# Kernel optimization log

Hardware: AMD Instinct MI355X
Metric: run time of the kernel (lower is better)

The kernel has to match this reference:

```python
import jax, jax.numpy as jnp
import numpy as np
import math

B, SEQ, E, H, NB, NHYP = 4, 1024, 512, 8, 64, 6
V, HID, NC, ENC = 32000, 2048, 6, 6
DH = E // H


def _pos_encoding(n, e, dtype):
    pos = jnp.arange(n, dtype=dtype)[:, None]
    div = jnp.exp(-jnp.arange(0, e, 2, dtype=dtype) * (math.log(10000.0) / e))
    ang = pos * div  # [n, e/2]
    pe = jnp.zeros((n, e), dtype)
    pe = pe.at[:, 0::2].set(jnp.sin(ang))
    pe = pe.at[:, 1::2].set(jnp.cos(ang))
    return pe


def _layer_norm(x, g, b):
    m = x.mean(-1, keepdims=True)
    v = ((x - m) ** 2).mean(-1, keepdims=True)
    return (x - m) / jnp.sqrt(v + 1e-5) * g + b


def _lsh_attention(x, Wq, bq, Wv, bv, hyper):
    b, n, e = x.shape
    q = x @ Wq + bq
    v = x @ Wv + bv
    q4 = q.reshape(b, n, H, DH)  # [b,n,h,d]
    v4 = v.reshape(b, n, H, DH)
    # bucket hashing: append bias 1, project on hyperplanes, binarize, binary-encode
    aug = jnp.concatenate([q4, jnp.ones((b, n, H, 1), q.dtype)], axis=-1)
    proj = jnp.einsum('bnhe,ey->bnhy', aug, hyper)
    bits = (proj >= 0).astype(q.dtype)
    pows = (2 ** jnp.arange(NHYP)).astype(q.dtype)
    buckets = jnp.einsum('bnhy,y->bnh', bits, pows).astype(jnp.int32)
    bh = buckets.transpose(0, 2, 1)  # [b,h,n]
    qh = q4.transpose(0, 2, 1, 3)  # [b,h,n,d]
    vh = v4.transpose(0, 2, 1, 3)
    scores = jnp.einsum('bhnd,bhmd->bhnm', qh, qh) / math.sqrt(e)
    # torch code zeroes q rows at their OWN bucket and sums q_c @ q_c^T over all
    # NB buckets; that equals scores * (NB - 2 + [bucket_i == bucket_j]) exactly.
    same = bh[:, :, :, None] == bh[:, :, None, :]
    count = (NB - 2 + same.astype(jnp.int32)).astype(scores.dtype)
    attn = jax.nn.softmax(scores * count, axis=-1)
    out = jnp.einsum('bhnm,bhmd->bhnd', attn, vh)
    return out.transpose(0, 2, 1, 3).reshape(b, n, e)


def setup_inputs() -> dict:
    key = jax.random.key(0)
    ks = jax.random.split(key, 16)
    s = 0.02
    emb = jax.random.normal(ks[0], (V, E), jnp.float32) * s
    emb = emb.at[V - 1].set(0.0)  # padding_idx row
    return dict(
        inputs=jax.random.randint(ks[1], (B, SEQ), 0, V),
        emb=emb,
        gamma=jnp.ones((E,), jnp.float32),
        beta=jnp.zeros((E,), jnp.float32),
        Wq=jax.random.normal(ks[2], (E, E), jnp.float32) * s,
        bq=jnp.zeros((E,), jnp.float32),
        Wv=jax.random.normal(ks[3], (E, E), jnp.float32) * s,
        bv=jnp.zeros((E,), jnp.float32),
        hyper=jax.random.normal(ks[4], (DH + 1, NHYP), jnp.float32),
        W1=jax.random.normal(ks[5], (E, HID), jnp.float32) * s,
        b1=jnp.zeros((HID,), jnp.float32),
        W2=jax.random.normal(ks[6], (HID, E), jnp.float32) * s,
        b2=jnp.zeros((E,), jnp.float32),
        Wm=jax.random.normal(ks[7], (E * SEQ, NC), jnp.float32) * 0.002,
        bm=jnp.zeros((NC,), jnp.float32),
    )


def reference(inputs, emb, gamma, beta, Wq, bq, Wv, bv, hyper, W1, b1, W2, b2, Wm, bm):
    x = emb[inputs]  # [B, SEQ, E]
    x = x + _pos_encoding(x.shape[1], x.shape[2], x.dtype)
    for _ in range(ENC):  # shared weights across encoders
        a = _lsh_attention(x, Wq, bq, Wv, bv, hyper)
        x = _layer_norm(a, gamma, beta)
        x = jax.nn.relu(x @ W1 + b1) @ W2 + b2 + x
        x = _layer_norm(x, gamma, beta)
    x = x.reshape(x.shape[0], -1)
    return x @ Wm + bm  # [B, NC]
```

## Files before the change

### kernel.cpp

```cpp
#include <hip/hip_runtime.h>
#include <hip/hip_bf16.h>
#include <math.h>

#define B_    4
#define SEQ_  1024
#define E_    512
#define H_    8
#define DH_   64
#define NHYP_ 6
#define HID_  2048
#define NC_   6
#define ENC_  6
#define BH_   (B_*H_)
#define NTOK_ 4096
#define NCAT_ 1088

typedef __attribute__((ext_vector_type(8))) short short8;
typedef __attribute__((ext_vector_type(4))) float f32x4;

static __device__ __forceinline__ float wave_rsum(float v){
#pragma unroll
  for(int o=32;o;o>>=1) v += __shfl_down(v,o,64);
  return v;
}
static __device__ __forceinline__ ushort f2b(float v){
  __hip_bfloat16 h = __float2bfloat16(v);
  return *(ushort*)&h;
}
static __device__ __forceinline__ float b2f(ushort u){
  unsigned int x = ((unsigned int)u) << 16;
  return *(float*)&x;
}
static __device__ __forceinline__ void gload16(const void* g, void* l){
  __builtin_amdgcn_global_load_lds(
      (const __attribute__((address_space(1))) void*)g,
      (__attribute__((address_space(3))) void*)l,
      16, 0, 0);
}

__global__ void embed_pe_kernel(const int* __restrict__ inp, const float* __restrict__ emb,
                                float* __restrict__ x, ushort* __restrict__ xh,
                                unsigned int* __restrict__ MaxN){
  int row = blockIdx.x;
  if(blockIdx.x==0 && threadIdx.x<32) MaxN[threadIdx.x] = 0u;
  int s = row & (SEQ_-1);
  int idx = inp[row];
  const float* er = emb + (size_t)idx*E_;
  float* xr = x + (size_t)row*E_;
  ushort* hr = xh + (size_t)row*E_;
  for(int c=threadIdx.x;c<E_;c+=blockDim.x){
    int i = c>>1;
    float div = expf(-(float)i * 0.0359778920780319646f);
    float ang = (float)s * div;
    float pe = (c&1) ? cosf(ang) : sinf(ang);
    float v = er[c] + pe;
    xr[c] = v;
    hr[c] = f2b(v);
  }
}

__global__ __launch_bounds__(256) void prep_kernel(
    const float* __restrict__ Wq, const float* __restrict__ Wv,
    const float* __restrict__ W1, const float* __restrict__ W2,
    const float* __restrict__ bq, const float* __restrict__ bv,
    const float* __restrict__ hyper,
    ushort* __restrict__ WcatT, ushort* __restrict__ W1T,
    ushort* __restrict__ W2T, float* __restrict__ bcat)
{
  int bid = blockIdx.x;
  if(bid < 2560){
    const float* W; ushort* Wt; int K, N, tile;
    if(bid < 256){       W=Wq; Wt=WcatT;                    K=512;  N=512;  tile=bid; }
    else if(bid < 512){  W=Wv; Wt=WcatT+(size_t)512*512;    K=512;  N=512;  tile=bid-256; }
    else if(bid < 1536){ W=W1; Wt=W1T;                      K=512;  N=2048; tile=bid-512; }
    else {               W=W2; Wt=W2T;                      K=2048; N=512;  tile=bid-1536; }
    int tpr = N >> 5;
    int n0 = (tile % tpr)*32, k0 = (tile / tpr)*32;
    __shared__ float T[32][33];
    int tx = threadIdx.x & 31, ty = threadIdx.x >> 5;
#pragma unroll
    for(int i=0;i<32;i+=8) T[ty+i][tx] = W[(size_t)(k0+ty+i)*N + n0+tx];
    __syncthreads();
#pragma unroll
    for(int i=0;i<32;i+=8)
      Wt[(size_t)(n0+ty+i)*K + k0+tx] = f2b(T[tx][ty+i]);
  } else if(bid < 2688){
    int t = (bid-2560)*256 + threadIdx.x;
    int c = t >> 9, k = t & 511;
    float s = 0.f;
    if(c < 48){
      int h = c/6, y = c%6;
      const float* wr = Wq + (size_t)k*E_ + h*DH_;
      for(int d=0;d<DH_;++d) s += wr[d]*hyper[d*NHYP_+y];
    }
    WcatT[(size_t)(1024+c)*E_ + k] = f2b(s);
  } else {
    int t = (bid-2688)*256 + threadIdx.x;
    if(t >= NCAT_) return;
    float v;
    if(t < 512) v = bq[t];
    else if(t < 1024) v = bv[t-512];
    else if(t < 1072){
      int c = t - 1024, h = c/6, y = c%6;
      float s = hyper[DH_*NHYP_ + y];
      for(int d=0;d<DH_;++d) s += bq[h*DH_+d]*hyper[d*NHYP_+y];
      v = s;
    } else v = 0.f;
    bcat[t] = v;
  }
}

template<int BM, int BN, int EPI>
__global__ __launch_bounds__(256) void gemm_mfma(
    const ushort* __restrict__ A, const ushort* __restrict__ Bt,
    const float* __restrict__ bias, const float* __restrict__ res,
    void* __restrict__ C0, void* __restrict__ C1, void* __restrict__ C2,
    void* __restrict__ C3, int M, int N, int K)
{
  constexpr int MI = BM/32, NI = BN/32;
  constexpr int ACH = BM/32, BCH = BN/32;
  __shared__ ushort As[2][BM*64];
  __shared__ ushort Bs[2][BN*64];
  __shared__ float epi[64*49];
  int tid = threadIdx.x;
  int w = tid>>6, lane = tid&63, g = lane>>4, li = lane&15;
  int wr = w>>1, wc = w&1;
  int bm = blockIdx.y*BM, bn = blockIdx.x*BN;
  int kz = blockIdx.z;
  int kcnt = K / (int)gridDim.z;
  int kbase = kz * kcnt;
  int NK = kcnt >> 6;

  f32x4 acc[MI][NI] = {};

  auto issue = [&](int ks, int pb){
    int k0 = kbase + ks*64;
#pragma unroll
    for(int it=0; it<ACH; ++it){
      int c = it*256 + tid; int r = c>>3; int kq = ((c&7)^(r&7))*8;
      gload16(&A[(size_t)(bm+r)*K + k0 + kq], &As[pb][it*2048 + w*512]);
    }
#pragma unroll
    for(int it=0; it<BCH; ++it){
      int c = it*256 + tid; int r = c>>3; int kq = ((c&7)^(r&7))*8;
      gload16(&Bt[(size_t)(bn+r)*K + k0 + kq], &Bs[pb][it*2048 + w*512]);
    }
  };

  issue(0, 0);
  __syncthreads();
  for(int ks=0; ks<NK; ++ks){
    if(ks+1 < NK) issue(ks+1, (ks+1)&1);
    int pb = ks&1;
#pragma unroll
    for(int kc=0; kc<2; ++kc){
      short8 af[MI], bf[NI];
#pragma unroll
      for(int mi=0;mi<MI;++mi)
        af[mi] = *(const short8*)&As[pb][(wr*(BM/2)+mi*16+li)*64 + (((kc*4+g)^(li&7))*8)];
#pragma unroll
      for(int ni=0;ni<NI;++ni)
        bf[ni] = *(const short8*)&Bs[pb][(wc*(BN/2)+ni*16+li)*64 + (((kc*4+g)^(li&7))*8)];
#pragma unroll
      for(int mi=0;mi<MI;++mi)
#pragma unroll
        for(int ni=0;ni<NI;++ni)
          acc[mi][ni] = __builtin_amdgcn_mfma_f32_16x16x32_bf16(af[mi], bf[ni], acc[mi][ni], 0,0,0);
    }
    __syncthreads();
  }

  if(EPI==5){
    if(bn < 512){
      int h = bn >> 6;
#pragma unroll
      for(int mi=0;mi<MI;++mi){
        int rbase = bm + wr*(BM/2) + mi*16 + g*4;
        float q2s[4] = {0.f,0.f,0.f,0.f};
#pragma unroll
        for(int ni=0;ni<NI;++ni){
          int cc = bn + wc*(BN/2) + ni*16 + li;
          float bv = bias[cc];
          int d = cc & 63;
#pragma unroll
          for(int j=0;j<4;++j){
            float vvf = acc[mi][ni][j] + bv;
            ushort ub = f2b(vvf);
            int r = rbase + j; int b = r>>10, n = r&1023;
            ((ushort*)C1)[(((size_t)(b*8+h))*1024 + n)*64 + d] = ub;
            float f = b2f(ub);
            q2s[j] += f*f;
          }
        }
#pragma unroll
        for(int j=0;j<4;++j){
#pragma unroll
          for(int o=8;o;o>>=1) q2s[j] += __shfl_xor(q2s[j], o, 64);
        }
        if(li==0){
#pragma unroll
          for(int j=0;j<4;++j)
            epi[(wr*(BM/2)+mi*16+g*4+j)*2 + wc] = q2s[j];
        }
      }
      __syncthreads();
      if(tid < 64){
        int r = bm + tid; int b = r>>10, n = r&1023;
        float q2 = epi[tid*2] + epi[tid*2+1];
        ((float*)C3)[((size_t)(b*8+h))*1024 + n] = q2;
        float m = q2;
#pragma unroll
        for(int o=32;o;o>>=1) m = fmaxf(m, __shfl_xor(m, o, 64));
        if(tid==0){
          int bh = (bm>>10)*8 + h;
          atomicMax((unsigned int*)res + bh, __float_as_uint(m));
        }
      }
    } else if(bn < 1024){
#pragma unroll
      for(int mi=0;mi<MI;++mi){
        int rbase = bm + wr*(BM/2) + mi*16 + g*4;
        int b = rbase>>10, n = rbase&1023;
#pragma unroll
        for(int ni=0;ni<NI;++ni){
          int cc = bn + wc*(BN/2) + ni*16 + li;
          float bv = bias[cc];
          int cl = cc - 512; int h = cl>>6, d = cl&63;
          ushort4 pk;
          pk.x = f2b(acc[mi][ni][0]+bv); pk.y = f2b(acc[mi][ni][1]+bv);
          pk.z = f2b(acc[mi][ni][2]+bv); pk.w = f2b(acc[mi][ni][3]+bv);
          *(ushort4*)&((ushort*)C2)[(((size_t)(b*8+h))*64 + d)*1024 + n] = pk;
        }
      }
    } else {
#pragma unroll
      for(int mi=0;mi<MI;++mi){
        int rloc = wr*(BM/2) + mi*16 + g*4;
#pragma unroll
        for(int ni=0;ni<NI;++ni){
          int c = wc*(BN/2) + ni*16 + li;
          if(c < 48){
            float bv = bias[1024 + c];
#pragma unroll
            for(int j=0;j<4;++j)
              epi[(rloc+j)*49 + c] = acc[mi][ni][j] + bv;
          }
        }
      }
      __syncthreads();
      if(tid < 64){
        int r = bm + tid; int b = r>>10, n = r&1023;
#pragma unroll
        for(int h=0;h<8;++h){
          int bk = 0;
#pragma unroll
          for(int y=0;y<NHYP_;++y)
            bk |= (epi[tid*49 + h*NHYP_ + y] >= 0.0f) ? (1<<y) : 0;
          ((int*)C0)[((size_t)(b*8+h))*1024 + n] = bk;
        }
      }
    }
    return;
  }

#pragma unroll
  for(int mi=0;mi<MI;++mi){
    int rbase = bm + wr*(BM/2) + mi*16 + g*4;
#pragma unroll
    for(int ni=0;ni<NI;++ni){
      int cc = bn + wc*(BN/2) + ni*16 + li;
      float bv = (EPI==6) ? 0.0f : bias[cc];
      float vv[4];
#pragma unroll
      for(int j=0;j<4;++j) vv[j] = acc[mi][ni][j] + bv;
      if(EPI==1){
#pragma unroll
        for(int j=0;j<4;++j) ((ushort*)C0)[(size_t)(rbase+j)*N + cc] = f2b(fmaxf(vv[j],0.0f));
      } else if(EPI==6){
        float* dst = (float*)C0 + (size_t)kz*M*N;
#pragma unroll
        for(int j=0;j<4;++j) dst[(size_t)(rbase+j)*N + cc] = vv[j];
      } else if(EPI==2){
#pragma unroll
        for(int j=0;j<4;++j){
          size_t o = (size_t)(rbase+j)*N + cc;
          ((float*)C0)[o] = vv[j] + res[o];
        }
      } else {
#pragma unroll
        for(int j=0;j<4;++j) ((float*)C0)[(size_t)(rbase+j)*N + cc] = vv[j];
      }
    }
  }
}

__global__ __launch_bounds__(256) void attn_mfma_kernel(
    const ushort* __restrict__ Qh,
    const ushort* __restrict__ Vt,
    const int* __restrict__ buckets,
    const float* __restrict__ qn2,
    const unsigned int* __restrict__ MaxN,
    float* __restrict__ outp)
{
  int bid = blockIdx.x;
  int bh = bid & 31;
  int qt = bid >> 5;
  int b = bh >> 3, h = bh & 7;
  int tid = threadIdx.x;
  int w = tid >> 6, lane = tid & 63;
  int g = lane >> 4, li = lane & 15;

  __shared__ ushort Ks[2][64*64];
  __shared__ ushort Vs[2][64*64];
  __shared__ ushort Ps[64*68];
  __shared__ int bks[2][64];
  __shared__ int bqs[64];

  const ushort* Qbase = Qh + (size_t)bh*SEQ_*DH_;
  const ushort* Vbase = Vt + (size_t)bh*DH_*SEQ_;
  const int* Bb = buckets + bh*SEQ_;
  const float* qn = qn2 + bh*SEQ_;
  int q0 = qt*64;

  auto issue = [&](int kt, int pb){
    int j0 = kt*64;
#pragma unroll
    for(int it=0; it<2; ++it){
      int c = it*256 + tid; int r = c>>3; int ks = ((c&7)^(r&7))*8;
      gload16(&Qbase[(size_t)(j0+r)*DH_ + ks], &Ks[pb][it*2048 + w*512]);
      gload16(&Vbase[(size_t)r*SEQ_ + j0 + ks], &Vs[pb][it*2048 + w*512]);
    }
    if(tid < 16) gload16(&Bb[j0 + tid*4], &bks[pb][0]);
  };

  issue(0, 0);
  short8 qa[2];
  int qrow = q0 + w*16 + li;
#pragma unroll
  for(int kc=0; kc<2; ++kc)
    qa[kc] = *(const short8*)&Qbase[(size_t)qrow*DH_ + kc*32 + g*8];
  if(tid < 64) bqs[tid] = Bb[q0 + tid];

  float maxn = sqrtf(__uint_as_float(MaxN[bh]));

  const float invsq = 0.04419417382415922f;
  const float LOG2E = 1.4426950408889634f;
  const float c62l = invsq * 62.0f * LOG2E;
  const float c63l = invsq * 63.0f * LOG2E;
  float nM2[4];
#pragma unroll
  for(int i=0;i<4;++i){
    float Mrow = invsq*63.0f * sqrtf(qn[q0 + w*16 + g*4 + i]) * maxn + 1.0f;
    nM2[i] = -Mrow * LOG2E;
  }
  __syncthreads();

  f32x4 acc_o[4] = {};
  float psum[4] = {0.f,0.f,0.f,0.f};

  for(int kt=0; kt<16; ++kt){
    if(kt < 15) issue(kt+1, (kt+1)&1);
    int pb = kt&1;

    f32x4 accs[4];
    __builtin_amdgcn_s_setprio(1);
#pragma unroll
    for(int nt=0; nt<4; ++nt){
      f32x4 z = {};
#pragma unroll
      for(int kc=0; kc<2; ++kc){
        short8 kb = *(const short8*)&Ks[pb][(nt*16+li)*64 + (((kc*4+g)^(li&7))*8)];
        z = __builtin_amdgcn_mfma_f32_16x16x32_bf16(qa[kc], kb, z, 0,0,0);
      }
      accs[nt] = z;
    }
    __builtin_amdgcn_s_setprio(0);
    int bkc[4];
#pragma unroll
    for(int nt=0;nt<4;++nt) bkc[nt] = bks[pb][nt*16 + li];

#pragma unroll
    for(int i=0;i<4;++i){
      int rloc = w*16 + g*4 + i;
      int bq = bqs[rloc];
      float rs = 0.f;
#pragma unroll
      for(int nt=0;nt<4;++nt){
        float cl = (bkc[nt] == bq) ? c63l : c62l;
        float e = exp2f(fmaf(accs[nt][i], cl, nM2[i]));
        rs += e;
        Ps[rloc*68 + nt*16 + li] = f2b(e);
      }
      psum[i] += rs;
    }
    __builtin_amdgcn_s_setprio(1);
#pragma unroll
    for(int dt=0; dt<4; ++dt){
      f32x4 z = acc_o[dt];
#pragma unroll
      for(int kc=0; kc<2; ++kc){
        short8 pa = *(const short8*)&Ps[(w*16+li)*68 + kc*32 + g*8];
        short8 vb = *(const short8*)&Vs[pb][(dt*16+li)*64 + (((kc*4+g)^(li&7))*8)];
        z = __builtin_amdgcn_mfma_f32_16x16x32_bf16(pa, vb, z, 0,0,0);
      }
      acc_o[dt] = z;
    }
    __builtin_amdgcn_s_setprio(0);
    __syncthreads();
  }
#pragma unroll
  for(int i=0;i<4;++i){
#pragma unroll
    for(int o=8;o;o>>=1) psum[i] += __shfl_xor(psum[i], o, 64);
  }
  float* obase = outp + ((size_t)(b*SEQ_ + q0 + w*16 + g*4))*E_ + h*DH_;
#pragma unroll
  for(int i=0;i<4;++i){
    float inv = 1.0f / fmaxf(psum[i], 1e-35f);
#pragma unroll
    for(int dt=0;dt<4;++dt)
      obase[(size_t)i*E_ + dt*16 + li] = acc_o[dt][i] * inv;
  }
}

__global__ __launch_bounds__(256) void ln_kernel(
    const float* __restrict__ in, const float* __restrict__ g,
    const float* __restrict__ bb, float* __restrict__ outp,
    ushort* __restrict__ oh, unsigned int* __restrict__ MaxN){
  if(blockIdx.x==0 && threadIdx.x<32) MaxN[threadIdx.x] = 0u;
  int row = blockIdx.x*4 + (threadIdx.x>>6);
  int lane = threadIdx.x & 63;
  const float4* xr = (const float4*)(in + (size_t)row*E_);
  float4 v0 = xr[lane*2], v1 = xr[lane*2+1];
  float s  = v0.x+v0.y+v0.z+v0.w + v1.x+v1.y+v1.z+v1.w;
  float s2 = v0.x*v0.x+v0.y*v0.y+v0.z*v0.z+v0.w*v0.w
           + v1.x*v1.x+v1.y*v1.y+v1.z*v1.z+v1.w*v1.w;
#pragma unroll
  for(int o=32;o;o>>=1){ s += __shfl_xor(s,o,64); s2 += __shfl_xor(s2,o,64); }
  float mean = s*(1.0f/E_);
  float var  = s2*(1.0f/E_) - mean*mean;
  float inv = rsqrtf(var + 1e-5f);
  const float4* g4 = (const float4*)(g) + lane*2;
  const float4* b4 = (const float4*)(bb) + lane*2;
  float4 g0 = g4[0], g1 = g4[1], b0 = b4[0], b1 = b4[1];
  float4 y0, y1;
  y0.x=(v0.x-mean)*inv*g0.x+b0.x; y0.y=(v0.y-mean)*inv*g0.y+b0.y;
  y0.z=(v0.z-mean)*inv*g0.z+b0.z; y0.w=(v0.w-mean)*inv*g0.w+b0.w;
  y1.x=(v1.x-mean)*inv*g1.x+b1.x; y1.y=(v1.y-mean)*inv*g1.y+b1.y;
  y1.z=(v1.z-mean)*inv*g1.z+b1.z; y1.w=(v1.w-mean)*inv*g1.w+b1.w;
  float4* orow = (float4*)(outp + (size_t)row*E_) + lane*2;
  orow[0] = y0; orow[1] = y1;
  ushort hs[8];
  hs[0]=f2b(y0.x); hs[1]=f2b(y0.y); hs[2]=f2b(y0.z); hs[3]=f2b(y0.w);
  hs[4]=f2b(y1.x); hs[5]=f2b(y1.y); hs[6]=f2b(y1.z); hs[7]=f2b(y1.w);
  *(uint4*)&oh[(size_t)row*E_ + lane*8] = *(uint4*)hs;
}

__global__ __launch_bounds__(256) void ln2_kernel(
    const float* __restrict__ P, const float* __restrict__ b2,
    const float* __restrict__ Xres, const float* __restrict__ g,
    const float* __restrict__ bb, float* __restrict__ outp,
    ushort* __restrict__ oh){
  int row = blockIdx.x*4 + (threadIdx.x>>6);
  int lane = threadIdx.x & 63;
  const float4* p0 = (const float4*)(P + (size_t)row*E_) + lane*2;
  const float4* p1 = (const float4*)(P + (size_t)NTOK_*E_ + (size_t)row*E_) + lane*2;
  const float4* xr = (const float4*)(Xres + (size_t)row*E_) + lane*2;
  const float4* c4 = (const float4*)(b2) + lane*2;
  float4 v0 = p0[0], v1 = p0[1], u0 = p1[0], u1 = p1[1];
  float4 x0 = xr[0], x1 = xr[1], cb0 = c4[0], cb1 = c4[1];
  v0.x += u0.x + cb0.x + x0.x; v0.y += u0.y + cb0.y + x0.y;
  v0.z += u0.z + cb0.z + x0.z; v0.w += u0.w + cb0.w + x0.w;
  v1.x += u1.x + cb1.x + x1.x; v1.y += u1.y + cb1.y + x1.y;
  v1.z += u1.z + cb1.z + x1.z; v1.w += u1.w + cb1.w + x1.w;
  float s  = v0.x+v0.y+v0.z+v0.w + v1.x+v1.y+v1.z+v1.w;
  float s2 = v0.x*v0.x+v0.y*v0.y+v0.z*v0.z+v0.w*v0.w
           + v1.x*v1.x+v1.y*v1.y+v1.z*v1.z+v1.w*v1.w;
#pragma unroll
  for(int o=32;o;o>>=1){ s += __shfl_xor(s,o,64); s2 += __shfl_xor(s2,o,64); }
  float mean = s*(1.0f/E_);
  float var  = s2*(1.0f/E_) - mean*mean;
  float inv = rsqrtf(var + 1e-5f);
  const float4* g4 = (const float4*)(g) + lane*2;
  const float4* b4 = (const float4*)(bb) + lane*2;
  float4 g0 = g4[0], g1 = g4[1], b0 = b4[0], b1 = b4[1];
  float4 y0, y1;
  y0.x=(v0.x-mean)*inv*g0.x+b0.x; y0.y=(v0.y-mean)*inv*g0.y+b0.y;
  y0.z=(v0.z-mean)*inv*g0.z+b0.z; y0.w=(v0.w-mean)*inv*g0.w+b0.w;
  y1.x=(v1.x-mean)*inv*g1.x+b1.x; y1.y=(v1.y-mean)*inv*g1.y+b1.y;
  y1.z=(v1.z-mean)*inv*g1.z+b1.z; y1.w=(v1.w-mean)*inv*g1.w+b1.w;
  float4* orow = (float4*)(outp + (size_t)row*E_) + lane*2;
  orow[0] = y0; orow[1] = y1;
  ushort hs[8];
  hs[0]=f2b(y0.x); hs[1]=f2b(y0.y); hs[2]=f2b(y0.z); hs[3]=f2b(y0.w);
  hs[4]=f2b(y1.x); hs[5]=f2b(y1.y); hs[6]=f2b(y1.z); hs[7]=f2b(y1.w);
  *(uint4*)&oh[(size_t)row*E_ + lane*8] = *(uint4*)hs;
}

__global__ void final_partial(const float* __restrict__ x, const float* __restrict__ Wm,
                              float* __restrict__ part){
  int b  = blockIdx.x >> 7;
  int ch = blockIdx.x & 127;
  const float* xb = x + (size_t)b*SEQ_*E_;
  int k0 = ch*4096;
  float acc[NC_] = {};
  for(int k=k0+threadIdx.x; k<k0+4096; k+=256){
    float xv = xb[k];
    const float* wrow = Wm + (size_t)k*NC_;
#pragma unroll
    for(int c=0;c<NC_;++c) acc[c] += xv*wrow[c];
  }
#pragma unroll
  for(int c=0;c<NC_;++c) acc[c] = wave_rsum(acc[c]);
  __shared__ float r[4][NC_];
  int w = threadIdx.x>>6, lane = threadIdx.x&63;
  if(lane==0){
#pragma unroll
    for(int c=0;c<NC_;++c) r[w][c] = acc[c];
  }
  __syncthreads();
  if(threadIdx.x==0){
#pragma unroll
    for(int c=0;c<NC_;++c)
      part[(size_t)blockIdx.x*NC_ + c] = r[0][c]+r[1][c]+r[2][c]+r[3][c];
  }
}

__global__ void final_reduce(const float* __restrict__ part, const float* __restrict__ bm,
                             float* __restrict__ out){
  int t = threadIdx.x;
  if(t >= B_*NC_) return;
  int b = t / NC_, c = t % NC_;
  float s = bm[c];
  for(int i=0;i<128;++i) s += part[(size_t)(b*128+i)*NC_ + c];
  out[t] = s;
}

extern "C" void kernel_launch(void* const* d_in, const int* in_sizes, int n_in,
                              void* d_out, int out_size, void* d_ws, size_t ws_size,
                              hipStream_t stream){
  const int*   inp   = (const int*)d_in[0];
  const float* emb   = (const float*)d_in[1];
  const float* gamma = (const float*)d_in[2];
  const float* beta  = (const float*)d_in[3];
  const float* Wq    = (const float*)d_in[4];
  const float* bq    = (const float*)d_in[5];
  const float* Wv    = (const float*)d_in[6];
  const float* bv    = (const float*)d_in[7];
  const float* hyper = (const float*)d_in[8];
  const float* W1    = (const float*)d_in[9];
  const float* b1    = (const float*)d_in[10];
  const float* W2    = (const float*)d_in[11];
  const float* b2    = (const float*)d_in[12];
  const float* Wm    = (const float*)d_in[13];
  const float* bm    = (const float*)d_in[14];
  float* out = (float*)d_out;

  char* ws = (char*)d_ws;
  size_t off = 0;
  auto alloc = [&](size_t bytes)->void*{
    void* p = ws + off; off += (bytes + 255) & ~(size_t)255; return p;
  };
  const size_t NTOK = (size_t)B_*SEQ_;
  float*  X    = (float*)alloc(NTOK*E_*sizeof(float));
  float*  A    = (float*)alloc(NTOK*E_*sizeof(float));
  float*  Op   = (float*)alloc((size_t)2*NTOK*E_*sizeof(float));
  ushort* Xh   = (ushort*)alloc(NTOK*E_*sizeof(ushort));
  ushort* Hh   = (ushort*)alloc(NTOK*HID_*sizeof(ushort));
  int*    Bk   = (int*)  alloc((size_t)BH_*SEQ_*sizeof(int));
  float*  Qn2  = (float*)alloc((size_t)BH_*SEQ_*sizeof(float));
  unsigned int* MaxN = (unsigned int*)alloc(32*sizeof(unsigned int));
  float*  Pp   = (float*)alloc((size_t)B_*128*NC_*sizeof(float));
  ushort* Qh   = (ushort*)alloc((size_t)BH_*SEQ_*DH_*sizeof(ushort));
  ushort* Vt   = (ushort*)alloc((size_t)BH_*DH_*SEQ_*sizeof(ushort));
  ushort* WcatT= (ushort*)alloc((size_t)NCAT_*E_*sizeof(ushort));
  ushort* W1T  = (ushort*)alloc((size_t)HID_*E_*sizeof(ushort));
  ushort* W2T  = (ushort*)alloc((size_t)E_*HID_*sizeof(ushort));
  float*  bcat = (float*)alloc(NCAT_*sizeof(float));
  (void)ws_size; (void)in_sizes; (void)n_in; (void)out_size;

  prep_kernel<<<2693, 256, 0, stream>>>(Wq, Wv, W1, W2, bq, bv, hyper,
                                        WcatT, W1T, W2T, bcat);
  embed_pe_kernel<<<B_*SEQ_, 256, 0, stream>>>(inp, emb, X, Xh, MaxN);

  dim3 gQV(NCAT_/64, (B_*SEQ_)/64);
  dim3 gF1(HID_/128, (B_*SEQ_)/128);
  dim3 gF2(E_/64,    (B_*SEQ_)/64, 2);
  for(int l=0;l<ENC_;++l){
    gemm_mfma<64,64,5><<<gQV, 256, 0, stream>>>(Xh, WcatT, bcat, (const float*)MaxN,
                                                Bk, Qh, Vt, Qn2, B_*SEQ_, NCAT_, E_);
    attn_mfma_kernel<<<BH_*16, 256, 0, stream>>>(Qh, Vt, Bk, Qn2, MaxN, A);
    ln_kernel<<<B_*SEQ_/4, 256, 0, stream>>>(A, gamma, beta, X, Xh, MaxN);
    gemm_mfma<128,128,1><<<gF1, 256, 0, stream>>>(Xh, W1T, b1, nullptr, Hh, nullptr, nullptr, nullptr, B_*SEQ_, HID_, E_);
    gemm_mfma<64,64,6><<<gF2, 256, 0, stream>>>(Hh, W2T, b2, nullptr, Op, nullptr, nullptr, nullptr, B_*SEQ_, E_, HID_);
    ln2_kernel<<<B_*SEQ_/4, 256, 0, stream>>>(Op, b2, X, gamma, beta, X, Xh);
  }
  final_partial<<<B_*128, 256, 0, stream>>>(X, Wm, Pp);
  final_reduce<<<1, 32, 0, stream>>>(Pp, bm, out);
}
```

Baseline: 596.5 us.

## Load attention K/V tiles directly from global memory instead of LDS staging

Removes the double-buffered LDS staging of K, V and key buckets in the attention kernel. Each wave now reads its MFMA operands and bucket ids straight from global memory, and query buckets are kept in registers. This drops the per-tile block barrier and the LDS traffic, but it also gives up the async prefetch overlap. Every wave now loads the full K/V tile redundantly, relying on L1/L2 hits and exposing global load latency inside the loop.

```diff
diff --git a/kernel.cpp b/kernel.cpp
--- a/kernel.cpp
+++ b/kernel.cpp
@@ -310,11 +310,7 @@
   int w = tid >> 6, lane = tid & 63;
   int g = lane >> 4, li = lane & 15;
 
-  __shared__ ushort Ks[2][64*64];
-  __shared__ ushort Vs[2][64*64];
   __shared__ ushort Ps[64*68];
-  __shared__ int bks[2][64];
-  __shared__ int bqs[64];
 
   const ushort* Qbase = Qh + (size_t)bh*SEQ_*DH_;
   const ushort* Vbase = Vt + (size_t)bh*DH_*SEQ_;
@@ -322,24 +318,11 @@
   const float* qn = qn2 + bh*SEQ_;
   int q0 = qt*64;
 
-  auto issue = [&](int kt, int pb){
-    int j0 = kt*64;
-#pragma unroll
-    for(int it=0; it<2; ++it){
-      int c = it*256 + tid; int r = c>>3; int ks = ((c&7)^(r&7))*8;
-      gload16(&Qbase[(size_t)(j0+r)*DH_ + ks], &Ks[pb][it*2048 + w*512]);
-      gload16(&Vbase[(size_t)r*SEQ_ + j0 + ks], &Vs[pb][it*2048 + w*512]);
-    }
-    if(tid < 16) gload16(&Bb[j0 + tid*4], &bks[pb][0]);
-  };
-
-  issue(0, 0);
   short8 qa[2];
   int qrow = q0 + w*16 + li;
 #pragma unroll
   for(int kc=0; kc<2; ++kc)
     qa[kc] = *(const short8*)&Qbase[(size_t)qrow*DH_ + kc*32 + g*8];
-  if(tid < 64) bqs[tid] = Bb[q0 + tid];
 
   float maxn = sqrtf(__uint_as_float(MaxN[bh]));
 
@@ -347,20 +330,20 @@
   const float LOG2E = 1.4426950408889634f;
   const float c62l = invsq * 62.0f * LOG2E;
   const float c63l = invsq * 63.0f * LOG2E;
-  float nM2[4];
+  float nM2[4]; int bqr[4];
 #pragma unroll
   for(int i=0;i<4;++i){
-    float Mrow = invsq*63.0f * sqrtf(qn[q0 + w*16 + g*4 + i]) * maxn + 1.0f;
+    int r = q0 + w*16 + g*4 + i;
+    float Mrow = invsq*63.0f * sqrtf(qn[r]) * maxn + 1.0f;
     nM2[i] = -Mrow * LOG2E;
-  }
-  __syncthreads();
+    bqr[i] = Bb[r];
+  }
 
   f32x4 acc_o[4] = {};
   float psum[4] = {0.f,0.f,0.f,0.f};
 
   for(int kt=0; kt<16; ++kt){
-    if(kt < 15) issue(kt+1, (kt+1)&1);
-    int pb = kt&1;
+    int j0 = kt*64;
 
     f32x4 accs[4];
     __builtin_amdgcn_s_setprio(1);
@@ -369,7 +352,7 @@
       f32x4 z = {};
 #pragma unroll
       for(int kc=0; kc<2; ++kc){
-        short8 kb = *(const short8*)&Ks[pb][(nt*16+li)*64 + (((kc*4+g)^(li&7))*8)];
+        short8 kb = *(const short8*)&Qbase[(size_t)(j0 + nt*16 + li)*DH_ + kc*32 + g*8];
         z = __builtin_amdgcn_mfma_f32_16x16x32_bf16(qa[kc], kb, z, 0,0,0);
       }
       accs[nt] = z;
@@ -377,12 +360,12 @@
     __builtin_amdgcn_s_setprio(0);
     int bkc[4];
 #pragma unroll
-    for(int nt=0;nt<4;++nt) bkc[nt] = bks[pb][nt*16 + li];
+    for(int nt=0;nt<4;++nt) bkc[nt] = Bb[j0 + nt*16 + li];
 
 #pragma unroll
     for(int i=0;i<4;++i){
       int rloc = w*16 + g*4 + i;
-      int bq = bqs[rloc];
+      int bq = bqr[i];
       float rs = 0.f;
 #pragma unroll
       for(int nt=0;nt<4;++nt){
@@ -400,13 +383,12 @@
 #pragma unroll
       for(int kc=0; kc<2; ++kc){
         short8 pa = *(const short8*)&Ps[(w*16+li)*68 + kc*32 + g*8];
-        short8 vb = *(const short8*)&Vs[pb][(dt*16+li)*64 + (((kc*4+g)^(li&7))*8)];
+        short8 vb = *(const short8*)&Vbase[(size_t)(dt*16 + li)*SEQ_ + j0 + kc*32 + g*8];
         z = __builtin_amdgcn_mfma_f32_16x16x32_bf16(pa, vb, z, 0,0,0);
       }
       acc_o[dt] = z;
     }
     __builtin_amdgcn_s_setprio(0);
-    __syncthreads();
   }
 #pragma unroll
   for(int i=0;i<4;++i){
```

Result: slower. 857.6 us (+43.8%).
